# Kernel optimization log

Hardware: AMD Instinct MI355X
Metric: run time of the kernel (lower is better)

## Reference

```python
import jax, jax.numpy as jnp
import numpy as np

V = 100000
NNZ = 1600000
B = 4
C_IN = 64
C_HID = 128
C_OUT = 64
K = 4
BN_EPS = 1e-5


def cheb_conv(x, rows, cols, vals, W, b):
    # x: (B, Cin, V); W: (K, Cin, Cout); b: (Cout,)
    Bn, Cin, Vn = x.shape
    Kn = W.shape[0]

    def spmm(y):  # y: (V, F) -> L @ y via edge-list scatter-add
        return jax.ops.segment_sum(vals[:, None] * y[cols], rows, num_segments=Vn)

    x0 = jnp.transpose(x, (2, 0, 1)).reshape(Vn, Bn * Cin)  # (V, B*Cin)
    xs = [x0]
    if Kn > 1:
        x1 = spmm(x0)
        xs.append(x1)
        for _ in range(2, Kn):
            x2 = 2.0 * spmm(x1) - x0  # Chebyshev recurrence
            xs.append(x2)
            x0, x1 = x1, x2
    Xk = jnp.stack(xs, 0).reshape(Kn, Vn, Bn, Cin)  # (K, V, B, Cin)
    out = jnp.einsum('kvbi,kio->bov', Xk, W)  # (B, Cout, V)
    return out + b[None, :, None]


def batch_norm(x, gamma, beta):
    # BatchNorm1d on (B, C, V): stats over (B, V), biased variance (training mode)
    mean = jnp.mean(x, axis=(0, 2), keepdims=True)
    var = jnp.mean(jnp.square(x - mean), axis=(0, 2), keepdims=True)
    xn = (x - mean) * jax.lax.rsqrt(var + BN_EPS)
    return xn * gamma[None, :, None] + beta[None, :, None]


def setup_inputs() -> dict:
    key = jax.random.key(0)
    ks = jax.random.split(key, 8)
    x = jax.random.normal(ks[0], (B, C_IN, V), dtype=jnp.float32)
    lap_rows = jax.random.randint(ks[1], (NNZ,), 0, V, dtype=jnp.int32)
    lap_cols = jax.random.randint(ks[2], (NNZ,), 0, V, dtype=jnp.int32)
    # scale so the effective Laplacian spectral norm is ~O(1) (Chebyshev assumes rescaled L)
    lap_vals = jax.random.normal(ks[3], (NNZ,), dtype=jnp.float32) * 0.01
    w1 = jax.random.normal(ks[4], (K, C_IN, C_HID), dtype=jnp.float32) * (1.0 / np.sqrt(K * C_IN))
    b1 = jnp.zeros((C_HID,), dtype=jnp.float32)
    bn_gamma = jnp.ones((C_HID,), dtype=jnp.float32)
    bn_beta = jnp.zeros((C_HID,), dtype=jnp.float32)
    w2 = jax.random.normal(ks[5], (K, C_HID, C_OUT), dtype=jnp.float32) * (1.0 / np.sqrt(K * C_HID))
    b2 = jnp.zeros((C_OUT,), dtype=jnp.float32)
    return {"x": x, "lap_rows": lap_rows, "lap_cols": lap_cols, "lap_vals": lap_vals,
            "w1": w1, "b1": b1, "bn_gamma": bn_gamma, "bn_beta": bn_beta,
            "w2": w2, "b2": b2}


def reference(x, lap_rows, lap_cols, lap_vals, w1, b1, bn_gamma, bn_beta, w2, b2):
    out = cheb_conv(x, lap_rows, lap_cols, lap_vals, w1, b1)
    out = jax.nn.relu(out)
    out = batch_norm(out, bn_gamma, bn_beta)
    out = cheb_conv(out, lap_rows, lap_cols, lap_vals, w2, b2)
    # in_channels == out_channels -> resizer is Identity
    return jax.nn.relu(out + x)
```

## Files before the change

### kernel.cpp

```cpp
#include <hip/hip_runtime.h>

#define V 100000
#define NNZ 1600000

typedef unsigned short ushort_t;
typedef unsigned int uint_t;
typedef __attribute__((ext_vector_type(4))) float f32x4;
typedef __attribute__((ext_vector_type(8))) short bf16x8;

__device__ __forceinline__ float bf2f(ushort_t u) {
    union { uint_t i; float f; } x; x.i = ((uint_t)u) << 16; return x.f;
}
__device__ __forceinline__ ushort_t f2bf(float f) {
    union { float f; uint_t i; } x; x.f = f;
    uint_t u = x.i;
    return (ushort_t)((u + 0x7fffu + ((u >> 16) & 1u)) >> 16);
}
__device__ __forceinline__ float blo(uint_t u) {
    union { uint_t i; float f; } x; x.i = u << 16; return x.f;
}
__device__ __forceinline__ float bhi(uint_t u) {
    union { uint_t i; float f; } x; x.i = u & 0xffff0000u; return x.f;
}

__global__ void diag_k(float* __restrict__ out, float code) {
    if (threadIdx.x == 0 && blockIdx.x == 0) out[0] = code;
}

__global__ __launch_bounds__(256) void pack_x0_k(const float* __restrict__ x,
                                                 ushort_t* __restrict__ x0) {
    __shared__ float tile[32][33];
    int v0 = blockIdx.x * 32, j0 = blockIdx.y * 32;
    int tx = threadIdx.x & 31, ty = threadIdx.x >> 5;
    for (int jj = ty; jj < 32; jj += 8)
        tile[jj][tx] = x[(size_t)(j0 + jj) * V + v0 + tx];
    __syncthreads();
    for (int vv = ty; vv < 32; vv += 8)
        x0[(size_t)(v0 + vv) * 256 + j0 + tx] = f2bf(tile[tx][vv]);
}

__global__ __launch_bounds__(256) void prep_w_k(const float* __restrict__ w1,
                                                const float* __restrict__ w2,
                                                ushort_t* __restrict__ wp1,
                                                ushort_t* __restrict__ wp2) {
    int idx = blockIdx.x * 256 + threadIdx.x;
    if (idx < 32768) {
        int f = idx;
        int j = f & 7, ch = (f >> 3) & 127, q = (f >> 10) & 3, kb = (f >> 12) & 3, L = (f >> 14) & 1;
        int k = kb * 32 + q * 8 + j;
        int t = L * 2 + (k >> 6), i = k & 63;
        wp1[idx] = f2bf(w1[((size_t)t * 64 + i) * 128 + ch]);
    } else {
        int f = idx - 32768;
        int j = f & 7, o = (f >> 3) & 63, q = (f >> 9) & 3, kb = (f >> 11) & 3, t = (f >> 13) & 3;
        int k = kb * 32 + q * 8 + j;
        wp2[f] = f2bf(w2[((size_t)t * 128 + k) * 64 + o]);
    }
}

__global__ __launch_bounds__(256) void hist_k(const int* __restrict__ rows,
                                              int* __restrict__ counts) {
    int e = blockIdx.x * 256 + threadIdx.x;
    atomicAdd(&counts[rows[e]], 1);
}

__global__ __launch_bounds__(256) void scan1_k(const int* __restrict__ counts,
                                               int* __restrict__ bsums) {
    __shared__ int sd[256];
    int t = threadIdx.x;
    int v = blockIdx.x * 256 + t;
    sd[t] = (v < V) ? counts[v] : 0;
    __syncthreads();
    for (int s = 128; s > 0; s >>= 1) {
        if (t < s) sd[t] += sd[t + s];
        __syncthreads();
    }
    if (t == 0) bsums[blockIdx.x] = sd[0];
}

__global__ __launch_bounds__(512) void scan2_k(int* __restrict__ bsums, int nb) {
    __shared__ int sd[512];
    int t = threadIdx.x;
    int v = (t < nb) ? bsums[t] : 0;
    sd[t] = v;
    __syncthreads();
    for (int off = 1; off < 512; off <<= 1) {
        int a = (t >= off) ? sd[t - off] : 0;
        __syncthreads();
        sd[t] += a;
        __syncthreads();
    }
    if (t < nb) bsums[t] = sd[t] - v;
}

__global__ __launch_bounds__(256) void scan3_k(const int* __restrict__ counts,
                                               const int* __restrict__ bsums,
                                               int* __restrict__ rowptr,
                                               int* __restrict__ cursor) {
    __shared__ int sd[256];
    int t = threadIdx.x;
    int v = blockIdx.x * 256 + t;
    int c = (v < V) ? counts[v] : 0;
    sd[t] = c;
    __syncthreads();
    for (int off = 1; off < 256; off <<= 1) {
        int a = (t >= off) ? sd[t - off] : 0;
        __syncthreads();
        sd[t] += a;
        __syncthreads();
    }
    if (v < V) {
        int start = bsums[blockIdx.x] + sd[t] - c;
        rowptr[v] = start;
        cursor[v] = start;
    }
    if (v == 0) rowptr[V] = NNZ;
}

__global__ __launch_bounds__(256) void scatter_k(const int* __restrict__ rows,
                                                 const int* __restrict__ cols,
                                                 const float* __restrict__ vals,
                                                 int* __restrict__ cursor,
                                                 int2* __restrict__ edges) {
    int e = blockIdx.x * 256 + threadIdx.x;
    int r = rows[e];
    int pos = atomicAdd(&cursor[r], 1);
    edges[pos] = make_int2(cols[e], __float_as_int(vals[e]));
}

__global__ __launch_bounds__(256) void spmm_wave(const int* __restrict__ rowptr,
                                                 const int2* __restrict__ edges,
                                                 const ushort_t* __restrict__ y,
                                                 const ushort_t* __restrict__ z,
                                                 float alpha, float beta,
                                                 ushort_t* __restrict__ out) {
    int v = (blockIdx.x * 256 + threadIdx.x) >> 6;
    if (v >= V) return;
    int l = threadIdx.x & 63;
    const ushort_t* yl = y + l * 4;

    float a0 = 0.f, a1 = 0.f, a2 = 0.f, a3 = 0.f;
    int e0 = rowptr[v], e1 = rowptr[v + 1];
    int e = e0;
    for (; e + 8 <= e1; e += 8) {
        int2 ed[8];
#pragma unroll
        for (int i = 0; i < 8; ++i) ed[i] = edges[e + i];
        uint2 u[8];
#pragma unroll
        for (int i = 0; i < 8; ++i) u[i] = *(const uint2*)(yl + (size_t)ed[i].x * 256);
#pragma unroll
        for (int i = 0; i < 8; ++i) {
            float wv = __int_as_float(ed[i].y);
            a0 += wv * blo(u[i].x);
            a1 += wv * bhi(u[i].x);
            a2 += wv * blo(u[i].y);
            a3 += wv * bhi(u[i].y);
        }
    }
    auto masked4 = [&](int base, int cnt) {
        int2 ed[4];
#pragma unroll
        for (int i = 0; i < 4; ++i) ed[i] = edges[i < cnt ? base + i : e0];
        uint2 u[4];
#pragma unroll
        for (int i = 0; i < 4; ++i) u[i] = *(const uint2*)(yl + (size_t)ed[i].x * 256);
#pragma unroll
        for (int i = 0; i < 4; ++i) {
            float wv = (i < cnt) ? __int_as_float(ed[i].y) : 0.f;
            a0 += wv * blo(u[i].x);
            a1 += wv * bhi(u[i].x);
            a2 += wv * blo(u[i].y);
            a3 += wv * bhi(u[i].y);
        }
    };
    int rem = e1 - e;
    if (rem > 0) masked4(e, rem > 4 ? 4 : rem);
    if (rem > 4) masked4(e + 4, rem - 4);

    float r0 = alpha * a0, r1 = alpha * a1, r2 = alpha * a2, r3 = alpha * a3;
    if (z) {
        uint2 t = *(const uint2*)(z + (size_t)v * 256 + l * 4);
        r0 += beta * blo(t.x);
        r1 += beta * bhi(t.x);
        r2 += beta * blo(t.y);
        r3 += beta * bhi(t.y);
    }
    uint2 st;
    st.x = (uint_t)f2bf(r0) | ((uint_t)f2bf(r1) << 16);
    st.y = (uint_t)f2bf(r2) | ((uint_t)f2bf(r3) << 16);
    *(uint2*)(out + (size_t)v * 256 + l * 4) = st;
}

__global__ __launch_bounds__(256) void gemm1_mfma(const ushort_t* __restrict__ t0,
                                                  const ushort_t* __restrict__ t1,
                                                  const ushort_t* __restrict__ wp,
                                                  const float* __restrict__ b1,
                                                  ushort_t* __restrict__ rb,
                                                  float* __restrict__ stats,
                                                  int first, int last) {
    __shared__ float s_sum[128];
    __shared__ float s_sq[128];
    int tid = threadIdx.x;
    int l = tid & 63, w = tid >> 6;
    int q = l >> 4, n16 = l & 15;
    int b = blockIdx.y;
    int v0 = blockIdx.x * 64;
    if (last && tid < 128) { s_sum[tid] = 0.f; s_sq[tid] = 0.f; }
    int vrow = v0 + w * 16 + n16;
    int vc = vrow < V ? vrow : V - 1;

    f32x4 acc[8];
#pragma unroll
    for (int ct = 0; ct < 8; ++ct) acc[ct] = (f32x4){0.f, 0.f, 0.f, 0.f};

#pragma unroll
    for (int kb = 0; kb < 4; ++kb) {
        const ushort_t* tab = (kb < 2) ? t0 : t1;
        bf16x8 a = *(const bf16x8*)(tab + (size_t)vc * 256 + b * 64 + (kb & 1) * 32 + q * 8);
#pragma unroll
        for (int ct = 0; ct < 8; ++ct) {
            bf16x8 bf = *(const bf16x8*)(wp + (size_t)(((kb * 4 + q) * 128) + ct * 16 + n16) * 8);
            acc[ct] = __builtin_amdgcn_mfma_f32_16x16x32_bf16(a, bf, acc[ct], 0, 0, 0);
        }
    }

    float ls[8], lq[8];
#pragma unroll
    for (int ct = 0; ct < 8; ++ct) {
        ls[ct] = 0.f; lq[ct] = 0.f;
        float bc = last ? b1[ct * 16 + n16] : 0.f;
#pragma unroll
        for (int r = 0; r < 4; ++r) {
            int v = v0 + w * 16 + q * 4 + r;
            bool valid = v < V;
            float val = acc[ct][r];
            ushort_t* p = rb + (size_t)(valid ? v : 0) * 512 + b * 128 + ct * 16 + n16;
            if (!first && valid) val += bf2f(*p);
            if (last) {
                val = fmaxf(val + bc, 0.f);
                if (valid) { ls[ct] += val; lq[ct] += val * val; }
            }
            if (valid) *p = f2bf(val);
        }
    }
    if (last) {
        __syncthreads();
#pragma unroll
        for (int ct = 0; ct < 8; ++ct) {
            atomicAdd(&s_sum[ct * 16 + n16], ls[ct]);
            atomicAdd(&s_sq[ct * 16 + n16], lq[ct]);
        }
        __syncthreads();
        if (tid < 128) {
            atomicAdd(&stats[tid], s_sum[tid]);
            atomicAdd(&stats[128 + tid], s_sq[tid]);
        }
    }
}

__global__ void finalize_k(const float* __restrict__ stats,
                           const float* __restrict__ gamma,
                           const float* __restrict__ beta,
                           float* __restrict__ ss) {
    int c = threadIdx.x;
    float n = (float)(4 * V);
    float mean = stats[c] / n;
    float var = stats[128 + c] / n - mean * mean;
    float inv = rsqrtf(var + 1e-5f);
    float sc = gamma[c] * inv;
    ss[c] = sc;
    ss[128 + c] = beta[c] - mean * sc;
}

__global__ __launch_bounds__(256) void gemmC_mfma(const ushort_t* __restrict__ rb,
                                                  const ushort_t* __restrict__ wp,
                                                  const ushort_t* __restrict__ S,
                                                  const float* __restrict__ ss,
                                                  ushort_t* __restrict__ P) {
    __shared__ float s_ss[256];
    int tid = threadIdx.x;
    s_ss[tid] = ss[tid];
    __syncthreads();
    int l = tid & 63, w = tid >> 6;
    int q = l >> 4, n16 = l & 15;
    int b = blockIdx.y;
    int v0 = blockIdx.x * 64;
    int vrow = v0 + w * 16 + n16;
    int vc = vrow < V ? vrow : V - 1;

    f32x4 acc[4];
#pragma unroll
    for (int ct = 0; ct < 4; ++ct) acc[ct] = (f32x4){0.f, 0.f, 0.f, 0.f};

#pragma unroll
    for (int kb = 0; kb < 4; ++kb) {
        int chl = kb * 32 + q * 8;
        bf16x8 a = *(const bf16x8*)(rb + (size_t)vc * 512 + b * 128 + chl);
#pragma unroll
        for (int j = 0; j < 8; ++j) {
            float f = bf2f((ushort_t)a[j]) * s_ss[chl + j] + s_ss[128 + chl + j];
            a[j] = (short)f2bf(f);
        }
#pragma unroll
        for (int ct = 0; ct < 4; ++ct) {
            bf16x8 bf = *(const bf16x8*)(wp + (size_t)(((kb * 4 + q) * 64) + ct * 16 + n16) * 8);
            acc[ct] = __builtin_amdgcn_mfma_f32_16x16x32_bf16(a, bf, acc[ct], 0, 0, 0);
        }
    }

#pragma unroll
    for (int ct = 0; ct < 4; ++ct) {
#pragma unroll
        for (int r = 0; r < 4; ++r) {
            int v = v0 + w * 16 + q * 4 + r;
            if (v < V) {
                size_t idx = (size_t)v * 256 + b * 64 + ct * 16 + n16;
                float val = acc[ct][r];
                if (S) val += bf2f(S[idx]);
                P[idx] = f2bf(val);
            }
        }
    }
}

__global__ __launch_bounds__(256) void gemm2_final(const ushort_t* __restrict__ rb,
                                                   const ushort_t* __restrict__ wp,
                                                   const ushort_t* __restrict__ Tb,
                                                   const float* __restrict__ b2,
                                                   const float* __restrict__ xres,
                                                   const float* __restrict__ ss,
                                                   float* __restrict__ out) {
    __shared__ float s_ss[256];
    int tid = threadIdx.x;
    s_ss[tid] = ss[tid];
    __syncthreads();
    int l = tid & 63, w = tid >> 6;
    int q = l >> 4, n16 = l & 15;
    int b = blockIdx.y;
    int v0 = blockIdx.x * 128;

    f32x4 acc[4][2];
#pragma unroll
    for (int rt = 0; rt < 4; ++rt)
#pragma unroll
        for (int c = 0; c < 2; ++c) acc[rt][c] = (f32x4){0.f, 0.f, 0.f, 0.f};

    int vcol[2];
#pragma unroll
    for (int c = 0; c < 2; ++c) {
        int v = v0 + (w * 2 + c) * 16 + n16;
        vcol[c] = v < V ? v : V - 1;
    }

#pragma unroll
    for (int kb = 0; kb < 4; ++kb) {
        int chl = kb * 32 + q * 8;
        bf16x8 bfr[2];
#pragma unroll
        for (int c = 0; c < 2; ++c) {
            bf16x8 t = *(const bf16x8*)(rb + (size_t)vcol[c] * 512 + b * 128 + chl);
#pragma unroll
            for (int j = 0; j < 8; ++j) {
                float f = bf2f((ushort_t)t[j]) * s_ss[chl + j] + s_ss[128 + chl + j];
                t[j] = (short)f2bf(f);
            }
            bfr[c] = t;
        }
#pragma unroll
        for (int rt = 0; rt < 4; ++rt) {
            bf16x8 af = *(const bf16x8*)(wp + (size_t)(((kb * 4 + q) * 64) + rt * 16 + n16) * 8);
#pragma unroll
            for (int c = 0; c < 2; ++c)
                acc[rt][c] = __builtin_amdgcn_mfma_f32_16x16x32_bf16(af, bfr[c], acc[rt][c], 0, 0, 0);
        }
    }

#pragma unroll
    for (int rt = 0; rt < 4; ++rt)
#pragma unroll
        for (int c = 0; c < 2; ++c) {
            int v = v0 + (w * 2 + c) * 16 + n16;
            bool valid = v < V;
#pragma unroll
            for (int r = 0; r < 4; ++r) {
                int o = rt * 16 + q * 4 + r;
                if (valid) {
                    size_t idx = (size_t)(b * 64 + o) * V + v;
                    float val = acc[rt][c][r] + bf2f(Tb[(size_t)v * 256 + b * 64 + o])
                              + b2[o] + xres[idx];
                    out[idx] = fmaxf(val, 0.f);
                }
            }
        }
}

extern "C" void kernel_launch(void* const* d_in, const int* in_sizes, int n_in,
                              void* d_out, int out_size, void* d_ws, size_t ws_size,
                              hipStream_t stream) {
    const float* x = (const float*)d_in[0];
    const int* lap_rows = (const int*)d_in[1];
    const int* lap_cols = (const int*)d_in[2];
    const float* lap_vals = (const float*)d_in[3];
    const float* w1 = (const float*)d_in[4];
    const float* b1 = (const float*)d_in[5];
    const float* bn_gamma = (const float*)d_in[6];
    const float* bn_beta = (const float*)d_in[7];
    const float* w2 = (const float*)d_in[8];
    const float* b2 = (const float*)d_in[9];
    float* out = (float*)d_out;

    char* ws = (char*)d_ws;
    size_t off = 0;
    auto alloc = [&](size_t bytes) {
        size_t r = off;
        off = (off + bytes + 255) & ~(size_t)255;
        return r;
    };
    size_t reg1_off = alloc((size_t)V * 512 * 2);
    size_t rb_off   = alloc((size_t)V * 512 * 2);
    size_t sc_off   = alloc((size_t)V * 256 * 2);
    size_t rp_off   = alloc((size_t)(V + 1) * 4);
    size_t cur_off  = alloc((size_t)V * 4);
    size_t ed_off   = alloc((size_t)NNZ * 8);
    size_t st_off   = alloc(256 * 4);
    size_t ss_off   = alloc(256 * 4);
    size_t bs_off   = alloc(512 * 4);
    size_t wp1_off  = alloc(32768 * 2);
    size_t wp2_off  = alloc(32768 * 2);

    if (ws_size < off) {
        diag_k<<<1, 64, 0, stream>>>(out, 1000.f + (float)(ws_size >> 20));
        return;
    }

    ushort_t* slotA = (ushort_t*)(ws + reg1_off);
    ushort_t* slotB = slotA + (size_t)V * 256;
    ushort_t* slotC = (ushort_t*)(ws + sc_off);
    ushort_t* rb = (ushort_t*)(ws + rb_off);
    int* rowptr = (int*)(ws + rp_off);
    int* cursor = (int*)(ws + cur_off);
    int2* edges = (int2*)(ws + ed_off);
    float* stats = (float*)(ws + st_off);
    float* ss = (float*)(ws + ss_off);
    int* bsums = (int*)(ws + bs_off);
    ushort_t* wp1 = (ushort_t*)(ws + wp1_off);
    ushort_t* wp2 = (ushort_t*)(ws + wp2_off);

    const int NB = (V + 255) / 256;
    const int SG = (V + 3) / 4;
    const ushort_t* nullu = (const ushort_t*)nullptr;

    hipMemsetAsync(cursor, 0, (size_t)V * 4, stream);
    hipMemsetAsync(stats, 0, 256 * 4, stream);

    pack_x0_k<<<dim3(V / 32, 8), 256, 0, stream>>>(x, slotA);
    prep_w_k<<<256, 256, 0, stream>>>(w1, w2, wp1, wp2);
    hist_k<<<NNZ / 256, 256, 0, stream>>>(lap_rows, cursor);
    scan1_k<<<NB, 256, 0, stream>>>(cursor, bsums);
    scan2_k<<<1, 512, 0, stream>>>(bsums, NB);
    scan3_k<<<NB, 256, 0, stream>>>(cursor, bsums, rowptr, cursor);
    scatter_k<<<NNZ / 256, 256, 0, stream>>>(lap_rows, lap_cols, lap_vals, cursor, edges);

    dim3 g1((V + 63) / 64, 4);
    dim3 g2((V + 127) / 128, 4);

    spmm_wave<<<SG, 256, 0, stream>>>(rowptr, edges, slotA, nullu, 1.f, 0.f, slotB);
    gemm1_mfma<<<g1, 256, 0, stream>>>(slotA, slotB, wp1, b1, rb, stats, 1, 0);
    spmm_wave<<<SG, 256, 0, stream>>>(rowptr, edges, slotB, slotA, 2.f, -1.f, slotA);
    spmm_wave<<<SG, 256, 0, stream>>>(rowptr, edges, slotA, slotB, 2.f, -1.f, slotB);
    gemm1_mfma<<<g1, 256, 0, stream>>>(slotA, slotB, wp1 + 16384, b1, rb, stats, 0, 1);

    finalize_k<<<1, 128, 0, stream>>>(stats, bn_gamma, bn_beta, ss);

    gemmC_mfma<<<g1, 256, 0, stream>>>(rb, wp2 + 3 * 8192, nullu, ss, slotA);
    spmm_wave<<<SG, 256, 0, stream>>>(rowptr, edges, slotA, nullu, 2.f, 0.f, slotB);
    gemmC_mfma<<<g1, 256, 0, stream>>>(rb, wp2 + 2 * 8192, slotB, ss, slotC);
    spmm_wave<<<SG, 256, 0, stream>>>(rowptr, edges, slotC, slotA, 2.f, -1.f, slotA);
    gemmC_mfma<<<g1, 256, 0, stream>>>(rb, wp2 + 1 * 8192, slotA, ss, slotB);
    spmm_wave<<<SG, 256, 0, stream>>>(rowptr, edges, slotB, slotC, 1.f, -1.f, slotC);
    gemm2_final<<<g2, 256, 0, stream>>>(rb, wp2, slotC, b2, x, ss, out);
}
```

Baseline: 1.638 ms.

## Stage GEMM epilogues through LDS for vectorized coalesced global stores

The three MFMA GEMM kernels now write their accumulators into shared memory and then reread them in row-contiguous chunks. This allows 16-byte vectorized bf16 loads and stores of the residual and partial buffers, plus float4 loads and stores for the final transposed output. It replaces the scattered 2-byte and 4-byte strided accesses of the MFMA lane layout. The BN statistics reduction also changes to wave shuffles followed by fewer shared-memory atomics. In exchange the kernels use much more LDS, which can lower occupancy, and they add extra barriers.

Result: faster. 1.505 ms (-8.1%).

```diff
diff --git a/kernel.cpp b/kernel.cpp
--- a/kernel.cpp
+++ b/kernel.cpp
@@ -21,6 +21,19 @@
 }
 __device__ __forceinline__ float bhi(uint_t u) {
     union { uint_t i; float f; } x; x.i = u & 0xffff0000u; return x.f;
+}
+__device__ __forceinline__ uint_t pk(float a, float b) {
+    return (uint_t)f2bf(a) | ((uint_t)f2bf(b) << 16);
+}
+__device__ __forceinline__ void unpack8(uint4 u, float* f) {
+    f[0] = blo(u.x); f[1] = bhi(u.x); f[2] = blo(u.y); f[3] = bhi(u.y);
+    f[4] = blo(u.z); f[5] = bhi(u.z); f[6] = blo(u.w); f[7] = bhi(u.w);
+}
+__device__ __forceinline__ uint4 pack8(const float* f) {
+    uint4 u;
+    u.x = pk(f[0], f[1]); u.y = pk(f[2], f[3]);
+    u.z = pk(f[4], f[5]); u.w = pk(f[6], f[7]);
+    return u;
 }
 
 __global__ void diag_k(float* __restrict__ out, float code) {
@@ -199,6 +212,7 @@
                                                   ushort_t* __restrict__ rb,
                                                   float* __restrict__ stats,
                                                   int first, int last) {
+    __shared__ float smem[64 * 130];
     __shared__ float s_sum[128];
     __shared__ float s_sq[128];
     int tid = threadIdx.x;
@@ -225,31 +239,68 @@
         }
     }
 
-    float ls[8], lq[8];
-#pragma unroll
-    for (int ct = 0; ct < 8; ++ct) {
-        ls[ct] = 0.f; lq[ct] = 0.f;
-        float bc = last ? b1[ct * 16 + n16] : 0.f;
-#pragma unroll
-        for (int r = 0; r < 4; ++r) {
-            int v = v0 + w * 16 + q * 4 + r;
-            bool valid = v < V;
-            float val = acc[ct][r];
-            ushort_t* p = rb + (size_t)(valid ? v : 0) * 512 + b * 128 + ct * 16 + n16;
-            if (!first && valid) val += bf2f(*p);
-            if (last) {
-                val = fmaxf(val + bc, 0.f);
-                if (valid) { ls[ct] += val; lq[ct] += val * val; }
+#pragma unroll
+    for (int ct = 0; ct < 8; ++ct)
+#pragma unroll
+        for (int r = 0; r < 4; ++r)
+            smem[(w * 16 + q * 4 + r) * 130 + ct * 16 + n16] = acc[ct][r];
+    __syncthreads();
+
+    int chunk = tid & 15;
+    int rbase = tid >> 4;
+    int ch0 = chunk * 8;
+    float bc[8];
+    if (last) {
+#pragma unroll
+        for (int j = 0; j < 8; ++j) bc[j] = b1[ch0 + j];
+    }
+    float csum[8], csq[8];
+#pragma unroll
+    for (int j = 0; j < 8; ++j) { csum[j] = 0.f; csq[j] = 0.f; }
+#pragma unroll
+    for (int k = 0; k < 4; ++k) {
+        int row = rbase + k * 16;
+        int v = v0 + row;
+        bool valid = v < V;
+        float vals[8];
+#pragma unroll
+        for (int j = 0; j < 8; ++j) vals[j] = smem[row * 130 + ch0 + j];
+        ushort_t* p = rb + (size_t)(valid ? v : 0) * 512 + b * 128 + ch0;
+        if (!first && valid) {
+            uint4 old = *(const uint4*)p;
+            float of[8];
+            unpack8(old, of);
+#pragma unroll
+            for (int j = 0; j < 8; ++j) vals[j] += of[j];
+        }
+        if (last) {
+#pragma unroll
+            for (int j = 0; j < 8; ++j) vals[j] = fmaxf(vals[j] + bc[j], 0.f);
+            if (valid) {
+#pragma unroll
+                for (int j = 0; j < 8; ++j) {
+                    csum[j] += vals[j];
+                    csq[j] += vals[j] * vals[j];
+                }
             }
-            if (valid) *p = f2bf(val);
-        }
-    }
+        }
+        if (valid) *(uint4*)p = pack8(vals);
+    }
+
     if (last) {
-        __syncthreads();
-#pragma unroll
-        for (int ct = 0; ct < 8; ++ct) {
-            atomicAdd(&s_sum[ct * 16 + n16], ls[ct]);
-            atomicAdd(&s_sq[ct * 16 + n16], lq[ct]);
+#pragma unroll
+        for (int j = 0; j < 8; ++j) {
+            csum[j] += __shfl_xor(csum[j], 16);
+            csum[j] += __shfl_xor(csum[j], 32);
+            csq[j] += __shfl_xor(csq[j], 16);
+            csq[j] += __shfl_xor(csq[j], 32);
+        }
+        if (l < 16) {
+#pragma unroll
+            for (int j = 0; j < 8; ++j) {
+                atomicAdd(&s_sum[ch0 + j], csum[j]);
+                atomicAdd(&s_sq[ch0 + j], csq[j]);
+            }
         }
         __syncthreads();
         if (tid < 128) {
@@ -279,6 +330,7 @@
                                                   const float* __restrict__ ss,
                                                   ushort_t* __restrict__ P) {
     __shared__ float s_ss[256];
+    __shared__ float smem[64 * 66];
     int tid = threadIdx.x;
     s_ss[tid] = ss[tid];
     __syncthreads();
@@ -310,17 +362,31 @@
     }
 
 #pragma unroll
-    for (int ct = 0; ct < 4; ++ct) {
-#pragma unroll
-        for (int r = 0; r < 4; ++r) {
-            int v = v0 + w * 16 + q * 4 + r;
-            if (v < V) {
-                size_t idx = (size_t)v * 256 + b * 64 + ct * 16 + n16;
-                float val = acc[ct][r];
-                if (S) val += bf2f(S[idx]);
-                P[idx] = f2bf(val);
-            }
-        }
+    for (int ct = 0; ct < 4; ++ct)
+#pragma unroll
+        for (int r = 0; r < 4; ++r)
+            smem[(w * 16 + q * 4 + r) * 66 + ct * 16 + n16] = acc[ct][r];
+    __syncthreads();
+
+#pragma unroll
+    for (int k = 0; k < 2; ++k) {
+        int seg = tid + k * 256;
+        int row = seg >> 3;
+        int o0 = (seg & 7) * 8;
+        int v = v0 + row;
+        if (v >= V) continue;
+        float vals[8];
+#pragma unroll
+        for (int j = 0; j < 8; ++j) vals[j] = smem[row * 66 + o0 + j];
+        size_t idx = (size_t)v * 256 + b * 64 + o0;
+        if (S) {
+            uint4 sv = *(const uint4*)(S + idx);
+            float sf[8];
+            unpack8(sv, sf);
+#pragma unroll
+            for (int j = 0; j < 8; ++j) vals[j] += sf[j];
+        }
+        *(uint4*)(P + idx) = pack8(vals);
     }
 }
 
@@ -332,13 +398,31 @@
                                                    const float* __restrict__ ss,
                                                    float* __restrict__ out) {
     __shared__ float s_ss[256];
+    __shared__ float smem[128 * 65];
     int tid = threadIdx.x;
     s_ss[tid] = ss[tid];
-    __syncthreads();
     int l = tid & 63, w = tid >> 6;
     int q = l >> 4, n16 = l & 15;
     int b = blockIdx.y;
     int v0 = blockIdx.x * 128;
+
+#pragma unroll
+    for (int k = 0; k < 4; ++k) {
+        int seg = tid + k * 256;
+        int row = seg >> 3;
+        int o0 = (seg & 7) * 8;
+        float tv[8];
+        if (v0 + row < V) {
+            uint4 t = *(const uint4*)(Tb + (size_t)(v0 + row) * 256 + b * 64 + o0);
+            unpack8(t, tv);
+        } else {
+#pragma unroll
+            for (int j = 0; j < 8; ++j) tv[j] = 0.f;
+        }
+#pragma unroll
+        for (int j = 0; j < 8; ++j) smem[row * 65 + o0 + j] = tv[j];
+    }
+    __syncthreads();
 
     f32x4 acc[4][2];
 #pragma unroll
@@ -380,19 +464,40 @@
     for (int rt = 0; rt < 4; ++rt)
 #pragma unroll
         for (int c = 0; c < 2; ++c) {
-            int v = v0 + (w * 2 + c) * 16 + n16;
-            bool valid = v < V;
-#pragma unroll
-            for (int r = 0; r < 4; ++r) {
-                int o = rt * 16 + q * 4 + r;
-                if (valid) {
-                    size_t idx = (size_t)(b * 64 + o) * V + v;
-                    float val = acc[rt][c][r] + bf2f(Tb[(size_t)v * 256 + b * 64 + o])
-                              + b2[o] + xres[idx];
-                    out[idx] = fmaxf(val, 0.f);
-                }
-            }
-        }
+            int vl = (w * 2 + c) * 16 + n16;
+#pragma unroll
+            for (int r = 0; r < 4; ++r)
+                acc[rt][c][r] += smem[vl * 65 + rt * 16 + q * 4 + r];
+        }
+    __syncthreads();
+
+#pragma unroll
+    for (int rt = 0; rt < 4; ++rt)
+#pragma unroll
+        for (int c = 0; c < 2; ++c) {
+            int vl = (w * 2 + c) * 16 + n16;
+#pragma unroll
+            for (int r = 0; r < 4; ++r)
+                smem[(rt * 16 + q * 4 + r) * 130 + vl] = acc[rt][c][r];
+        }
+    __syncthreads();
+
+    int o = tid >> 2, m = tid & 3;
+    float bias = b2[o];
+    const float* xr = xres + (size_t)(b * 64 + o) * V + v0;
+    float* op = out + (size_t)(b * 64 + o) * V + v0;
+#pragma unroll
+    for (int j = 0; j < 8; ++j) {
+        int voff = m * 4 + j * 16;
+        if (v0 + voff < V) {
+            f32x4 xv = *(const f32x4*)(xr + voff);
+            f32x4 res;
+#pragma unroll
+            for (int i = 0; i < 4; ++i)
+                res[i] = fmaxf(smem[o * 130 + voff + i] + bias + xv[i], 0.f);
+            *(f32x4*)(op + voff) = res;
+        }
+    }
 }
 
 extern "C" void kernel_launch(void* const* d_in, const int* in_sizes, int n_in,
```
